# Kernel optimization log

Hardware: AMD Instinct MI355X
Metric: run time of the kernel (lower is better)

The kernel has to match this reference:

```python
import jax, jax.numpy as jnp
import numpy as np

N, E, D = 20000, 320000, 256
EPS = 1e-5


def setup_inputs() -> dict:
    key = jax.random.key(0)
    ks = jax.random.split(key, 12)
    s = 1.0 / np.sqrt(D)
    s2 = 1.0 / np.sqrt(2 * D)
    return {
        "node_embeddings": jax.random.normal(ks[0], (N, D), jnp.float32),
        "edge_index": jax.random.randint(ks[1], (2, E), 0, N, jnp.int64),
        "edge_embeddings": jax.random.normal(ks[2], (E, D), jnp.float32),
        # message MLP: Linear(D,D) -> GELU -> Linear(D,D)
        "W1m": jax.random.uniform(ks[3], (D, D), jnp.float32, -s, s),
        "b1m": jnp.zeros((D,), jnp.float32),
        "W2m": jax.random.uniform(ks[4], (D, D), jnp.float32, -s, s),
        "b2m": jnp.zeros((D,), jnp.float32),
        # update MLP: Linear(D,2D) -> GELU -> Linear(2D,D)
        "W1u": jax.random.uniform(ks[5], (D, 2 * D), jnp.float32, -s, s),
        "b1u": jnp.zeros((2 * D,), jnp.float32),
        "W2u": jax.random.uniform(ks[6], (2 * D, D), jnp.float32, -s2, s2),
        "b2u": jnp.zeros((D,), jnp.float32),
        # LayerNorm params
        "gamma": jnp.ones((D,), jnp.float32),
        "beta": jnp.zeros((D,), jnp.float32),
    }


def _layer_norm(x, gamma, beta):
    mu = jnp.mean(x, axis=-1, keepdims=True)
    var = jnp.mean(jnp.square(x - mu), axis=-1, keepdims=True)
    return (x - mu) * jax.lax.rsqrt(var + EPS) * gamma + beta


def reference(node_embeddings, edge_index, edge_embeddings,
              W1m, b1m, W2m, b2m, W1u, b1u, W2u, b2u, gamma, beta):
    src = edge_index[0]
    dst = edge_index[1]
    n = node_embeddings.shape[0]
    # gather + edge add + message MLP (exact erf GELU, as torch default)
    h = node_embeddings[src] + edge_embeddings           # [E, D]
    h = jax.nn.gelu(h @ W1m + b1m, approximate=False)
    messages = h @ W2m + b2m                             # [E, D]
    # scatter-mean aggregation
    agg = jax.ops.segment_sum(messages, dst, num_segments=n)  # [N, D]
    deg = jax.ops.segment_sum(jnp.ones((dst.shape[0], 1), node_embeddings.dtype),
                              dst, num_segments=n)            # [N, 1]
    agg = agg / jnp.maximum(deg, 1.0)
    # update MLP + residual + LayerNorm
    u = jax.nn.gelu(agg @ W1u + b1u, approximate=False) @ W2u + b2u
    return _layer_norm(node_embeddings + u, gamma, beta)
```

## Files before the change

### kernel.cpp

```cpp
#include <hip/hip_runtime.h>
#include <hip/hip_bf16.h>

#define N_NODES 20000
#define N_EDGES 320000
#define EBLK 64
#define NBLK 32

typedef __attribute__((ext_vector_type(8))) short short8;
typedef __attribute__((ext_vector_type(4))) float f32x4;

static __device__ __forceinline__ unsigned short f2bf(float f) {
  __hip_bfloat16 h = __float2bfloat16(f);
  union { __hip_bfloat16 h; unsigned short u; } cv; cv.h = h; return cv.u;
}

static __device__ __forceinline__ float bf2f(unsigned short u) {
  union { unsigned int u; float f; } cv; cv.u = ((unsigned int)u) << 16; return cv.f;
}

static __device__ __forceinline__ unsigned int pk2(float a, float b) {
  return (unsigned int)f2bf(a) | ((unsigned int)f2bf(b) << 16);
}

static __device__ __forceinline__ float gelu_f(float x) {
  float z = x * (2.3022082f + 0.1029432f * x * x);
  z = fminf(fmaxf(z, -30.0f), 30.0f);
  float t = exp2f(z);
  return x * t * __frcp_rn(1.0f + t);
}

#define SWZ(row, byteoff) ((byteoff) ^ (((row) & 7) << 4))
#define SWZU(b) ((b) ^ ((((b) >> 8) & 7) << 4))

__global__ void packhist_kernel(const float* __restrict__ W1m, const float* __restrict__ W2m,
                                const float* __restrict__ W1u, const float* __restrict__ W2u,
                                unsigned short* __restrict__ P1m, unsigned short* __restrict__ P2m,
                                unsigned short* __restrict__ P1u, unsigned short* __restrict__ P2u,
                                const int* __restrict__ dst, int* __restrict__ cnt) {
  if (blockIdx.x >= 1536) {
    int e = (blockIdx.x - 1536) * blockDim.x + threadIdx.x;
    atomicAdd(&cnt[dst[e]], 1);
    return;
  }
  int idx = blockIdx.x * blockDim.x + threadIdx.x;
  const float* W; unsigned short* P; int K, Nc, local;
  if (idx < 65536)        { W = W1m; P = P1m; K = 256; Nc = 256; local = idx; }
  else if (idx < 131072)  { W = W2m; P = P2m; K = 256; Nc = 256; local = idx - 65536; }
  else if (idx < 262144)  { W = W1u; P = P1u; K = 256; Nc = 512; local = idx - 131072; }
  else                    { W = W2u; P = P2u; K = 512; Nc = 256; local = idx - 262144; }
  int frag = local >> 9, wi = local & 511;
  int l = wi >> 3, i = wi & 7;
  int kf = K >> 5;
  int cf = frag / kf, t = frag % kf;
  int k = t * 32 + (l >> 4) * 8 + i;
  int n = cf * 16 + (l & 15);
  P[local] = f2bf(W[(size_t)k * Nc + n]);
}

__global__ __launch_bounds__(1024) void scan_kernel(const int* __restrict__ cnt,
                                                    int* __restrict__ rptr,
                                                    int* __restrict__ cur) {
  __shared__ int wsum[16];
  const int t = threadIdx.x;
  const int lane = t & 63, wid = t >> 6;
  const int base = t * 20;
  int local[20];
  int s = 0;
#pragma unroll
  for (int i = 0; i < 20; ++i) {
    int idx = base + i;
    int v = (idx < N_NODES) ? cnt[idx] : 0;
    local[i] = s;
    s += v;
  }
  int x = s;
#pragma unroll
  for (int off = 1; off < 64; off <<= 1) {
    int v = __shfl_up(x, off);
    if (lane >= off) x += v;
  }
  if (lane == 63) wsum[wid] = x;
  __syncthreads();
  if (t < 16) {
    int y = wsum[t];
#pragma unroll
    for (int off = 1; off < 16; off <<= 1) {
      int v = __shfl_up(y, off);
      if (t >= off) y += v;
    }
    wsum[t] = y;
  }
  __syncthreads();
  const int woff = (wid > 0) ? wsum[wid - 1] : 0;
  const int incl = x + woff;
  const int excl = incl - s;
#pragma unroll
  for (int i = 0; i < 20; ++i) {
    int idx = base + i;
    if (idx < N_NODES) { int p = excl + local[i]; rptr[idx] = p; cur[idx] = p; }
  }
  if (t == 1023) rptr[N_NODES] = incl;
}

__global__ __launch_bounds__(256, 4) void scatnw1_kernel(
    const int* __restrict__ dst, int* __restrict__ cur, int* __restrict__ perm,
    const float* __restrict__ node, const unsigned short* __restrict__ P1m,
    const float* __restrict__ b1m, unsigned short* __restrict__ NW1) {
  __shared__ unsigned short tA[NBLK * 256];
  const int tid = threadIdx.x;
  if (blockIdx.x < 1250) {
    int e = blockIdx.x * 256 + tid;
    int d = dst[e];
    int pos = atomicAdd(&cur[d], 1);
    perm[pos] = e;
    return;
  }
  const int n0 = (blockIdx.x - 1250) * NBLK;
  {
    const int r = tid >> 3;
    const int cs = (tid & 7) * 32;
    const float* np = node + (size_t)(n0 + r) * 256 + cs;
#pragma unroll
    for (int i = 0; i < 4; ++i) {
      float4 a = *(const float4*)(np + i * 8);
      float4 b = *(const float4*)(np + i * 8 + 4);
      uint4 p;
      p.x = pk2(a.x, a.y); p.y = pk2(a.z, a.w);
      p.z = pk2(b.x, b.y); p.w = pk2(b.z, b.w);
      *(uint4*)((char*)tA + SWZ(r, r * 512 + (cs + i * 8) * 2)) = p;
    }
  }
  __syncthreads();
  const int w = tid >> 6, l = tid & 63, lr = l & 15, lh = l >> 4;
  f32x4 acc[2][4];
#pragma unroll
  for (int r4 = 0; r4 < 2; ++r4)
#pragma unroll
    for (int c = 0; c < 4; ++c) acc[r4][c] = f32x4{0.f, 0.f, 0.f, 0.f};
#pragma unroll
  for (int t = 0; t < 8; ++t) {
    const int row0 = lr, row1 = 16 + lr;
    short8 af0 = *(const short8*)((const char*)tA + SWZ(row0, row0 * 512 + t * 64 + lh * 16));
    short8 af1 = *(const short8*)((const char*)tA + SWZ(row1, row1 * 512 + t * 64 + lh * 16));
#pragma unroll
    for (int c = 0; c < 4; ++c) {
      short8 bfr = *(const short8*)(P1m + (size_t)(((w * 4 + c) * 8 + t) * 512 + l * 8));
      acc[0][c] = __builtin_amdgcn_mfma_f32_16x16x32_bf16(af0, bfr, acc[0][c], 0, 0, 0);
      acc[1][c] = __builtin_amdgcn_mfma_f32_16x16x32_bf16(af1, bfr, acc[1][c], 0, 0, 0);
    }
  }
#pragma unroll
  for (int r4 = 0; r4 < 2; ++r4)
#pragma unroll
    for (int c = 0; c < 4; ++c) {
      int col = w * 64 + c * 16 + lr;
      float bb = b1m[col];
#pragma unroll
      for (int j = 0; j < 4; ++j) {
        int row = r4 * 16 + lh * 4 + j;
        NW1[(size_t)(n0 + row) * 256 + col] = f2bf(acc[r4][c][j] + bb);
      }
    }
}

__global__ __launch_bounds__(512, 7) void edge_kernel(
    const float* __restrict__ eemb,
    const int* __restrict__ src, const int* __restrict__ dst,
    const int* __restrict__ perm,
    const unsigned short* __restrict__ P1m, const unsigned short* __restrict__ NW1,
    float* __restrict__ S) {
  __shared__ unsigned short tA[EBLK * 256];
  __shared__ int dstS[EBLK], srcS[EBLK];
  const int tid = threadIdx.x;
  const int e0 = blockIdx.x * EBLK;
  {
    const int r = tid >> 3;
    const int cs = (tid & 7) * 32;
    const int e = perm[e0 + r];
    if ((tid & 7) == 0) { dstS[r] = dst[e]; srcS[r] = src[e]; }
    const float* ep = eemb + (size_t)e * 256 + cs;
#pragma unroll
    for (int i = 0; i < 4; ++i) {
      float4 a = *(const float4*)(ep + i * 8);
      float4 b = *(const float4*)(ep + i * 8 + 4);
      uint4 p;
      p.x = pk2(a.x, a.y); p.y = pk2(a.z, a.w);
      p.z = pk2(b.x, b.y); p.w = pk2(b.z, b.w);
      *(uint4*)((char*)tA + SWZ(r, r * 512 + (cs + i * 8) * 2)) = p;
    }
  }
  __syncthreads();

  const int w = tid >> 6, l = tid & 63;
  const int lr = l & 15, lh = l >> 4;
  const int colbase = w * 32 + lr;

  unsigned short nw0[4][4], nw1[4][4];
#pragma unroll
  for (int r4 = 0; r4 < 4; ++r4)
#pragma unroll
    for (int j = 0; j < 4; ++j) {
      int row = r4 * 16 + lh * 4 + j;
      const unsigned short* nwp = NW1 + (size_t)srcS[row] * 256 + colbase;
      nw0[r4][j] = nwp[0];
      nw1[r4][j] = nwp[16];
    }

  f32x4 acc[4][2];
#pragma unroll
  for (int r4 = 0; r4 < 4; ++r4)
#pragma unroll
    for (int c = 0; c < 2; ++c) acc[r4][c] = f32x4{0.f, 0.f, 0.f, 0.f};
#pragma unroll
  for (int kt = 0; kt < 8; ++kt) {
    short8 af[4];
#pragma unroll
    for (int r4 = 0; r4 < 4; ++r4) {
      int row = r4 * 16 + lr;
      af[r4] = *(const short8*)((const char*)tA + SWZ(row, row * 512 + kt * 64 + lh * 16));
    }
#pragma unroll
    for (int c = 0; c < 2; ++c) {
      short8 bfr = *(const short8*)(P1m + (size_t)(((w * 2 + c) * 8 + kt) * 512 + l * 8));
#pragma unroll
      for (int r4 = 0; r4 < 4; ++r4)
        acc[r4][c] = __builtin_amdgcn_mfma_f32_16x16x32_bf16(af[r4], bfr, acc[r4][c], 0, 0, 0);
    }
  }

#pragma unroll
  for (int r4 = 0; r4 < 4; ++r4)
#pragma unroll
    for (int j = 0; j < 4; ++j) {
      acc[r4][0][j] = gelu_f(acc[r4][0][j] + bf2f(nw0[r4][j]));
      acc[r4][1][j] = gelu_f(acc[r4][1][j] + bf2f(nw1[r4][j]));
    }

  const int dv = dstS[l];
  const int pv = __shfl(dv, (l - 1) & 63);
  const bool bflag = (l == 0) || (dv != pv);
  const unsigned long long mask = __ballot(bflag);
  const int nseg = __popcll(mask);
  int sid[4][4];
#pragma unroll
  for (int r4 = 0; r4 < 4; ++r4)
#pragma unroll
    for (int j = 0; j < 4; ++j) {
      int row = r4 * 16 + lh * 4 + j;
      sid[r4][j] = __popcll(mask & ((2ULL << row) - 1)) - 1;
    }
  unsigned long long rem = mask;
  for (int s = 0; s < nseg; ++s) {
    const int rowf = __builtin_ctzll(rem);
    rem &= rem - 1;
    const int dseg = __shfl(dv, rowf);
    float p0 = 0.f, p1 = 0.f;
#pragma unroll
    for (int r4 = 0; r4 < 4; ++r4)
#pragma unroll
      for (int j = 0; j < 4; ++j) {
        bool m = (sid[r4][j] == s);
        p0 += m ? acc[r4][0][j] : 0.f;
        p1 += m ? acc[r4][1][j] : 0.f;
      }
    p0 += __shfl_xor(p0, 16); p0 += __shfl_xor(p0, 32);
    p1 += __shfl_xor(p1, 16); p1 += __shfl_xor(p1, 32);
    if (lh == 0) {
      float* Sp = S + (size_t)dseg * 256 + colbase;
      atomicAdd(Sp, p0);
      atomicAdd(Sp + 16, p1);
    }
  }
}

__global__ __launch_bounds__(256, 4) void node_kernel(
    const float* __restrict__ node, const float* __restrict__ S, const int* __restrict__ rptr,
    const unsigned short* __restrict__ P2m, const float* __restrict__ b2m,
    const unsigned short* __restrict__ P1u, const float* __restrict__ b1u,
    const unsigned short* __restrict__ P2u, const float* __restrict__ b2u,
    const float* __restrict__ gamma, const float* __restrict__ beta,
    float* __restrict__ out) {
  __shared__ unsigned short tAB[2][NBLK * 256];
  __shared__ unsigned short tH[NBLK * 256];
  __shared__ float fmu[NBLK], frs[NBLK], fflag[NBLK];
  float* tU = (float*)tAB;
  const int tid = threadIdx.x;
  const int n0 = blockIdx.x * NBLK;
  const int r = tid >> 3;
  const int cs = (tid & 7) * 32;
  const int n = n0 + r;
  {
    int dgi = rptr[n + 1] - rptr[n];
    float rec = 1.0f / fmaxf((float)dgi, 1.0f);
    if ((tid & 7) == 0) fflag[r] = (dgi > 0) ? 1.0f : 0.0f;
    const float* sp = S + (size_t)n * 256 + cs;
#pragma unroll
    for (int i = 0; i < 4; ++i) {
      float4 a = *(const float4*)(sp + i * 8);
      float4 b = *(const float4*)(sp + i * 8 + 4);
      uint4 p;
      p.x = pk2(a.x * rec, a.y * rec);
      p.y = pk2(a.z * rec, a.w * rec);
      p.z = pk2(b.x * rec, b.y * rec);
      p.w = pk2(b.z * rec, b.w * rec);
      *(uint4*)((char*)tAB[0] + SWZ(r, r * 512 + (cs + i * 8) * 2)) = p;
    }
  }
  __syncthreads();
  const int w = tid >> 6, l = tid & 63, lr = l & 15, lh = l >> 4;

  {
    f32x4 acc[2][4];
#pragma unroll
    for (int r4 = 0; r4 < 2; ++r4)
#pragma unroll
      for (int c = 0; c < 4; ++c) acc[r4][c] = f32x4{0.f, 0.f, 0.f, 0.f};
#pragma unroll
    for (int t = 0; t < 8; ++t) {
      const int row0 = lr, row1 = 16 + lr;
      short8 af0 = *(const short8*)((const char*)tAB[0] + SWZ(row0, row0 * 512 + t * 64 + lh * 16));
      short8 af1 = *(const short8*)((const char*)tAB[0] + SWZ(row1, row1 * 512 + t * 64 + lh * 16));
#pragma unroll
      for (int c = 0; c < 4; ++c) {
        short8 bfr = *(const short8*)(P2m + (size_t)(((w * 4 + c) * 8 + t) * 512 + l * 8));
        acc[0][c] = __builtin_amdgcn_mfma_f32_16x16x32_bf16(af0, bfr, acc[0][c], 0, 0, 0);
        acc[1][c] = __builtin_amdgcn_mfma_f32_16x16x32_bf16(af1, bfr, acc[1][c], 0, 0, 0);
      }
    }
#pragma unroll
    for (int r4 = 0; r4 < 2; ++r4)
#pragma unroll
      for (int c = 0; c < 4; ++c) {
        int col = w * 64 + c * 16 + lr;
        float bm = b2m[col];
#pragma unroll
        for (int j = 0; j < 4; ++j) {
          int row = r4 * 16 + lh * 4 + j;
          float v = acc[r4][c][j] + fflag[row] * bm;
          *(unsigned short*)((char*)tAB[1] + SWZ(row, row * 512 + col * 2)) = f2bf(v);
        }
      }
  }
  __syncthreads();

  f32x4 acc3[2][4];
#pragma unroll
  for (int c = 0; c < 4; ++c) {
    float bb = b2u[w * 64 + c * 16 + lr];
    acc3[0][c] = f32x4{bb, bb, bb, bb};
    acc3[1][c] = f32x4{bb, bb, bb, bb};
  }
#pragma unroll
  for (int half = 0; half < 2; ++half) {
    {
      f32x4 acc[2][4];
#pragma unroll
      for (int r4 = 0; r4 < 2; ++r4)
#pragma unroll
        for (int c = 0; c < 4; ++c) acc[r4][c] = f32x4{0.f, 0.f, 0.f, 0.f};
#pragma unroll
      for (int t = 0; t < 8; ++t) {
        const int row0 = lr, row1 = 16 + lr;
        short8 af0 = *(const short8*)((const char*)tAB[1] + SWZ(row0, row0 * 512 + t * 64 + lh * 16));
        short8 af1 = *(const short8*)((const char*)tAB[1] + SWZ(row1, row1 * 512 + t * 64 + lh * 16));
#pragma unroll
        for (int c = 0; c < 4; ++c) {
          short8 bfr = *(const short8*)(P1u + (size_t)(((half * 16 + w * 4 + c) * 8 + t) * 512 + l * 8));
          acc[0][c] = __builtin_amdgcn_mfma_f32_16x16x32_bf16(af0, bfr, acc[0][c], 0, 0, 0);
          acc[1][c] = __builtin_amdgcn_mfma_f32_16x16x32_bf16(af1, bfr, acc[1][c], 0, 0, 0);
        }
      }
#pragma unroll
      for (int r4 = 0; r4 < 2; ++r4)
#pragma unroll
        for (int c = 0; c < 4; ++c) {
          int col = w * 64 + c * 16 + lr;
          float b1 = b1u[half * 256 + col];
#pragma unroll
          for (int j = 0; j < 4; ++j) {
            int row = r4 * 16 + lh * 4 + j;
            float v = gelu_f(acc[r4][c][j] + b1);
            *(unsigned short*)((char*)tH + SWZ(row, row * 512 + col * 2)) = f2bf(v);
          }
        }
    }
    __syncthreads();
    {
#pragma unroll
      for (int tt = 0; tt < 8; ++tt) {
        const int row0 = lr, row1 = 16 + lr;
        short8 af0 = *(const short8*)((const char*)tH + SWZ(row0, row0 * 512 + tt * 64 + lh * 16));
        short8 af1 = *(const short8*)((const char*)tH + SWZ(row1, row1 * 512 + tt * 64 + lh * 16));
#pragma unroll
        for (int c = 0; c < 4; ++c) {
          short8 bfr = *(const short8*)(P2u + (size_t)(((w * 4 + c) * 16 + half * 8 + tt) * 512 + l * 8));
          acc3[0][c] = __builtin_amdgcn_mfma_f32_16x16x32_bf16(af0, bfr, acc3[0][c], 0, 0, 0);
          acc3[1][c] = __builtin_amdgcn_mfma_f32_16x16x32_bf16(af1, bfr, acc3[1][c], 0, 0, 0);
        }
      }
    }
    __syncthreads();
  }

#pragma unroll
  for (int r4 = 0; r4 < 2; ++r4)
#pragma unroll
    for (int c = 0; c < 4; ++c) {
      int col = w * 64 + c * 16 + lr;
#pragma unroll
      for (int j = 0; j < 4; ++j) {
        int row = r4 * 16 + lh * 4 + j;
        *(float*)((char*)tU + SWZU(row * 1024 + col * 4)) = acc3[r4][c][j];
      }
    }
  __syncthreads();

  {
    float sum = 0.f, sq = 0.f;
#pragma unroll
    for (int i = 0; i < 8; ++i) {
      int byte = SWZU(r * 1024 + (cs + i * 4) * 4);
      float4 v = *(float4*)((char*)tU + byte);
      const float4 nb = *(const float4*)(node + (size_t)n * 256 + cs + i * 4);
      v.x += nb.x; v.y += nb.y; v.z += nb.z; v.w += nb.w;
      *(float4*)((char*)tU + byte) = v;
      sum += v.x + v.y + v.z + v.w;
      sq += v.x * v.x + v.y * v.y + v.z * v.z + v.w * v.w;
    }
    sum += __shfl_xor(sum, 1); sum += __shfl_xor(sum, 2); sum += __shfl_xor(sum, 4);
    sq  += __shfl_xor(sq, 1);  sq  += __shfl_xor(sq, 2);  sq  += __shfl_xor(sq, 4);
    if ((tid & 7) == 0) {
      float mu = sum * (1.0f / 256.0f);
      fmu[r] = mu;
      frs[r] = rsqrtf(fmaxf(sq * (1.0f / 256.0f) - mu * mu, 0.0f) + 1e-5f);
    }
  }
  __syncthreads();
#pragma unroll
  for (int i = 0; i < 8; ++i) {
    int f4 = i * 256 + tid;
    int row = f4 >> 6;
    int c4 = f4 & 63;
    float4 v = *(float4*)((char*)tU + SWZU(row * 1024 + c4 * 16));
    float mu = fmu[row], rs = frs[row];
    float4 g  = *(const float4*)(gamma + c4 * 4);
    float4 bt = *(const float4*)(beta + c4 * 4);
    float4 o;
    o.x = (v.x - mu) * rs * g.x + bt.x;
    o.y = (v.y - mu) * rs * g.y + bt.y;
    o.z = (v.z - mu) * rs * g.z + bt.z;
    o.w = (v.w - mu) * rs * g.w + bt.w;
    *(float4*)(out + (size_t)(n0 + row) * 256 + c4 * 4) = o;
  }
}

extern "C" void kernel_launch(void* const* d_in, const int* in_sizes, int n_in,
                              void* d_out, int out_size, void* d_ws, size_t ws_size,
                              hipStream_t stream) {
  const float* node = (const float*)d_in[0];
  const int* eidx = (const int*)d_in[1];
  const float* eemb = (const float*)d_in[2];
  const float* W1m = (const float*)d_in[3];
  const float* b1m = (const float*)d_in[4];
  const float* W2m = (const float*)d_in[5];
  const float* b2m = (const float*)d_in[6];
  const float* W1u = (const float*)d_in[7];
  const float* b1u = (const float*)d_in[8];
  const float* W2u = (const float*)d_in[9];
  const float* b2u = (const float*)d_in[10];
  const float* gamma = (const float*)d_in[11];
  const float* beta = (const float*)d_in[12];
  float* out = (float*)d_out;

  char* ws = (char*)d_ws;
  int* cnt  = (int*)ws;
  int* rptr = (int*)(ws + 81920);
  int* cur  = (int*)(ws + 163840);
  int* perm = (int*)(ws + 245760);
  unsigned short* P1m = (unsigned short*)(ws + 1525760);
  unsigned short* P2m = (unsigned short*)(ws + 1656832);
  unsigned short* P1u = (unsigned short*)(ws + 1787904);
  unsigned short* P2u = (unsigned short*)(ws + 2050048);
  unsigned short* NW1 = (unsigned short*)(ws + 2312192);
  const int* src = eidx;
  const int* dst = eidx + N_EDGES;

  hipMemsetAsync(out, 0, (size_t)N_NODES * 256 * 4, stream);
  hipMemsetAsync(cnt, 0, (size_t)N_NODES * 4, stream);
  packhist_kernel<<<1536 + 1250, 256, 0, stream>>>(W1m, W2m, W1u, W2u,
                                                   P1m, P2m, P1u, P2u, dst, cnt);
  scan_kernel<<<1, 1024, 0, stream>>>(cnt, rptr, cur);
  scatnw1_kernel<<<1250 + 625, 256, 0, stream>>>(dst, cur, perm, node, P1m, b1m, NW1);
  edge_kernel<<<N_EDGES / EBLK, 512, 0, stream>>>(eemb, src, dst, perm, P1m, NW1, out);
  node_kernel<<<N_NODES / NBLK, 256, 0, stream>>>(node, out, rptr, P2m, b2m,
                                                  P1u, b1u, P2u, b2u, gamma, beta, out);
}
```

Before: 310.5 us.

## Segment-reduce edge messages with a one-hot MFMA and simplify GELU

When a 64-edge block spans at most 16 destination segments, the messages are staged transposed in LDS as bf16. A one-hot segment matrix built from per-row segment ids is multiplied against them with MFMA, replacing the per-segment masked-sum and shuffle loop before the atomics. Blocks with more than 16 segments fall back to the old loop. The sigmoid-form GELU is also rewritten to avoid one multiply. In exchange, messages are rounded to bf16 before aggregation and two extra block-wide syncs are added.

```diff
diff --git a/kernel.cpp b/kernel.cpp
--- a/kernel.cpp
+++ b/kernel.cpp
@@ -8,6 +8,8 @@
 
 typedef __attribute__((ext_vector_type(8))) short short8;
 typedef __attribute__((ext_vector_type(4))) float f32x4;
+typedef __attribute__((ext_vector_type(8))) unsigned char uchar8;
+typedef __attribute__((ext_vector_type(4))) unsigned short ushort4v;
 
 static __device__ __forceinline__ unsigned short f2bf(float f) {
   __hip_bfloat16 h = __float2bfloat16(f);
@@ -23,13 +25,14 @@
 }
 
 static __device__ __forceinline__ float gelu_f(float x) {
-  float z = x * (2.3022082f + 0.1029432f * x * x);
-  z = fminf(fmaxf(z, -30.0f), 30.0f);
-  float t = exp2f(z);
-  return x * t * __frcp_rn(1.0f + t);
+  float w = -2.3022082f - 0.1029432f * x * x;
+  float zneg = fminf(x * w, 126.0f);
+  float t = exp2f(zneg);
+  return x * __frcp_rn(1.0f + t);
 }
 
 #define SWZ(row, byteoff) ((byteoff) ^ (((row) & 7) << 4))
+#define SWZT(col, byteoff) ((byteoff) ^ (((col) & 7) << 4))
 #define SWZU(b) ((b) ^ ((((b) >> 8) & 7) << 4))
 
 __global__ void packhist_kernel(const float* __restrict__ W1m, const float* __restrict__ W2m,
@@ -171,6 +174,8 @@
     float* __restrict__ S) {
   __shared__ unsigned short tA[EBLK * 256];
   __shared__ int dstS[EBLK], srcS[EBLK];
+  __shared__ unsigned char sidRowL[64];
+  __shared__ int dsegL[16];
   const int tid = threadIdx.x;
   const int e0 = blockIdx.x * EBLK;
   {
@@ -241,34 +246,85 @@
   const bool bflag = (l == 0) || (dv != pv);
   const unsigned long long mask = __ballot(bflag);
   const int nseg = __popcll(mask);
-  int sid[4][4];
-#pragma unroll
-  for (int r4 = 0; r4 < 4; ++r4)
-#pragma unroll
-    for (int j = 0; j < 4; ++j) {
-      int row = r4 * 16 + lh * 4 + j;
-      sid[r4][j] = __popcll(mask & ((2ULL << row) - 1)) - 1;
-    }
-  unsigned long long rem = mask;
-  for (int s = 0; s < nseg; ++s) {
-    const int rowf = __builtin_ctzll(rem);
-    rem &= rem - 1;
-    const int dseg = __shfl(dv, rowf);
-    float p0 = 0.f, p1 = 0.f;
+
+  if (nseg <= 16) {
+    if (w == 0) {
+      int sl = __popcll(mask & ((2ULL << l) - 1)) - 1;
+      sidRowL[l] = (unsigned char)sl;
+      if (bflag) dsegL[sl] = dv;
+    }
+    __syncthreads();
+
+#pragma unroll
+    for (int c = 0; c < 2; ++c) {
+      int col = w * 32 + c * 16 + lr;
+#pragma unroll
+      for (int r4 = 0; r4 < 4; ++r4) {
+        ushort4v v;
+        v.x = f2bf(acc[r4][c][0]); v.y = f2bf(acc[r4][c][1]);
+        v.z = f2bf(acc[r4][c][2]); v.w = f2bf(acc[r4][c][3]);
+        int byte0 = col * 128 + r4 * 32 + lh * 8;
+        *(ushort4v*)((char*)tA + SWZT(col, byte0)) = v;
+      }
+    }
+    __syncthreads();
+
+    uchar8 s0 = *(const uchar8*)(sidRowL + lh * 8);
+    uchar8 s1 = *(const uchar8*)(sidRowL + 32 + lh * 8);
+    short8 ia0, ia1;
+#pragma unroll
+    for (int i = 0; i < 8; ++i) {
+      ia0[i] = (s0[i] == lr) ? (short)0x3F80 : (short)0;
+      ia1[i] = (s1[i] == lr) ? (short)0x3F80 : (short)0;
+    }
+    f32x4 d[2] = {f32x4{0.f, 0.f, 0.f, 0.f}, f32x4{0.f, 0.f, 0.f, 0.f}};
+#pragma unroll
+    for (int c = 0; c < 2; ++c) {
+      int col = w * 32 + c * 16 + lr;
+      short8 b0 = *(const short8*)((const char*)tA + SWZT(col, col * 128 + lh * 16));
+      short8 b1 = *(const short8*)((const char*)tA + SWZT(col, col * 128 + 64 + lh * 16));
+      d[c] = __builtin_amdgcn_mfma_f32_16x16x32_bf16(ia0, b0, d[c], 0, 0, 0);
+      d[c] = __builtin_amdgcn_mfma_f32_16x16x32_bf16(ia1, b1, d[c], 0, 0, 0);
+    }
+#pragma unroll
+    for (int c = 0; c < 2; ++c) {
+      int col = w * 32 + c * 16 + lr;
+#pragma unroll
+      for (int j = 0; j < 4; ++j) {
+        int s = lh * 4 + j;
+        if (s < nseg) atomicAdd(S + (size_t)dsegL[s] * 256 + col, d[c][j]);
+      }
+    }
+  } else {
+    int sid[4][4];
 #pragma unroll
     for (int r4 = 0; r4 < 4; ++r4)
 #pragma unroll
       for (int j = 0; j < 4; ++j) {
-        bool m = (sid[r4][j] == s);
-        p0 += m ? acc[r4][0][j] : 0.f;
-        p1 += m ? acc[r4][1][j] : 0.f;
-      }
-    p0 += __shfl_xor(p0, 16); p0 += __shfl_xor(p0, 32);
-    p1 += __shfl_xor(p1, 16); p1 += __shfl_xor(p1, 32);
-    if (lh == 0) {
-      float* Sp = S + (size_t)dseg * 256 + colbase;
-      atomicAdd(Sp, p0);
-      atomicAdd(Sp + 16, p1);
+        int row = r4 * 16 + lh * 4 + j;
+        sid[r4][j] = __popcll(mask & ((2ULL << row) - 1)) - 1;
+      }
+    unsigned long long rem = mask;
+    for (int s = 0; s < nseg; ++s) {
+      const int rowf = __builtin_ctzll(rem);
+      rem &= rem - 1;
+      const int dseg = __shfl(dv, rowf);
+      float p0 = 0.f, p1 = 0.f;
+#pragma unroll
+      for (int r4 = 0; r4 < 4; ++r4)
+#pragma unroll
+        for (int j = 0; j < 4; ++j) {
+          bool m = (sid[r4][j] == s);
+          p0 += m ? acc[r4][0][j] : 0.f;
+          p1 += m ? acc[r4][1][j] : 0.f;
+        }
+      p0 += __shfl_xor(p0, 16); p0 += __shfl_xor(p0, 32);
+      p1 += __shfl_xor(p1, 16); p1 += __shfl_xor(p1, 32);
+      if (lh == 0) {
+        float* Sp = S + (size_t)dseg * 256 + colbase;
+        atomicAdd(Sp, p0);
+        atomicAdd(Sp + 16, p1);
+      }
     }
   }
 }
```

After: 331.3 us. +6.7%, slower.
